# Kernel optimization log

Measured on AMD Instinct MI355X. Metric: run time of the kernel, lower is better.

## Reference

```python
import jax, jax.numpy as jnp
import numpy as np

B, L, D = 8, 128, 512
MAW = 8             # config.max_arg_width
SWF = 20            # config.span_width_feature_size
FF = 512            # config.ffnn_size
R = 19              # label_space_size - 1
G = 4               # gold predicates per sentence
SPAN = 3 * D + SWF  # span_emb_size = 1556


def setup_inputs() -> dict:
    key = jax.random.key(0)
    ks = jax.random.split(key, 30)
    w = lambda k, shape, s=0.02: (jax.random.normal(k, shape, dtype=jnp.float32) * s)
    z = lambda n: jnp.zeros((n,), jnp.float32)
    return {
        'hidden_states': jax.random.normal(ks[0], (B, L, D), dtype=jnp.float32),
        'sent_lengths': 64 + jax.random.randint(ks[1], (B,), 0, L - 64 + 1),
        'gold_predicates': jax.random.randint(ks[2], (B, G), 0, 64),
        'width_emb_table': w(ks[3], (MAW, SWF), 0.1),
        'arg_w0': w(ks[4], (SPAN, FF)), 'arg_b0': z(FF),
        'arg_w1': w(ks[5], (FF, FF)), 'arg_b1': z(FF),
        'arg_wp': w(ks[6], (FF, 1)), 'arg_bp': z(1),
        'pred_w0': w(ks[7], (D, FF)), 'pred_b0': z(FF),
        'pred_w1': w(ks[8], (FF, FF)), 'pred_b1': z(FF),
        'pred_wp': w(ks[9], (FF, 1)), 'pred_bp': z(1),
        'srl_w0': w(ks[10], (SPAN + D, FF)), 'srl_b0': z(FF),
        'srl_w1': w(ks[11], (FF, FF)), 'srl_b1': z(FF),
        'srl_wp': w(ks[12], (FF, R)), 'srl_bp': z(R),
        'scale_w': w(ks[13], (D, SPAN)), 'scale_b': z(SPAN),
        'biaffine_w': w(ks[14], (R, SPAN + 1, SPAN + 1), 0.005),
    }


def _ffn(x, w0, b0, w1, b1, wp, bp):
    # stacked Linear+ReLU (dropout = identity at inference) + projection
    h = jax.nn.relu(x @ w0 + b0)
    h = jax.nn.relu(h @ w1 + b1)
    return h @ wp + bp


def reference(hidden_states, sent_lengths, gold_predicates, width_emb_table,
              arg_w0, arg_b0, arg_w1, arg_b1, arg_wp, arg_bp,
              pred_w0, pred_b0, pred_w1, pred_b1, pred_wp, pred_bp,
              srl_w0, srl_b0, srl_w1, srl_b1, srl_wp, srl_bp,
              scale_w, scale_b, biaffine_w):
    S = L * MAW  # candidates per sentence
    # --- get_candidate_spans: note original flattening order is [width, start] ---
    starts = jnp.broadcast_to(jnp.arange(L), (B, MAW, L)).reshape(B, S)
    widths = jnp.broadcast_to(jnp.arange(MAW)[None, :, None], (B, MAW, L)).reshape(B, S)
    ends = starts + widths
    cand_mask = ends < sent_lengths[:, None]            # [B, S]
    starts = starts * cand_mask
    ends = ends * cand_mask
    # --- get_span_emb: gathers of start/end tokens, width embedding, head mean ---
    b_idx = jnp.arange(B)[:, None]
    start_emb = hidden_states[b_idx, starts]            # [B, S, D]
    end_emb = hidden_states[b_idx, ends]                # [B, S, D]
    width_idx = ends - starts                           # span_width - 1
    width_emb = width_emb_table[width_idx]              # [B, S, SWF]
    span_idx = jnp.clip(starts[:, :, None] + jnp.arange(MAW), 0, L - 1)  # [B, S, MAW]
    text_emb = hidden_states[jnp.arange(B)[:, None, None], span_idx]     # [B, S, MAW, D]
    idx_mask = (jnp.arange(MAW) <= width_idx[:, :, None]).astype(hidden_states.dtype)
    head_emb = jnp.mean(text_emb * idx_mask[..., None], axis=2)  # mean over MAW (as torch.mean)
    span_emb = jnp.concatenate([start_emb, end_emb, width_emb, head_emb], axis=-1)  # [B, S, SPAN]
    # --- arg unary scores ---
    arg_scores = _ffn(span_emb, arg_w0, arg_b0, arg_w1, arg_b1, arg_wp, arg_bp)[..., 0]  # [B, S]
    # --- gold predicates: gather token embeddings, pred unary scores ---
    pred_emb = hidden_states[b_idx, gold_predicates]    # [B, G, D]
    pred_scores = _ffn(pred_emb, pred_w0, pred_b0, pred_w1, pred_b1, pred_wp, pred_bp)[..., 0]  # [B, G]
    # --- SRL pairwise FFN on concat(span_emb, pred_emb); split first layer to avoid
    #     materializing the [B,S,G,SPAN+D] concat (same math) ---
    a = span_emb @ srl_w0[:SPAN]                        # [B, S, FF]
    p = pred_emb @ srl_w0[SPAN:]                        # [B, G, FF]
    h = jax.nn.relu(a[:, :, None, :] + p[:, None, :, :] + srl_b0)  # [B, S, G, FF]
    h = jax.nn.relu(h @ srl_w1 + srl_b1)
    srl_unary = h @ srl_wp + srl_bp                     # [B, S, G, R]
    # --- biaffine: predicate_scale FeedForward then bilinear with bias on both sides ---
    pred_scaled = jax.nn.relu(pred_emb @ scale_w + scale_b)  # [B, G, SPAN]
    ones_s = jnp.ones(span_emb.shape[:-1] + (1,), span_emb.dtype)
    ones_p = jnp.ones(pred_scaled.shape[:-1] + (1,), pred_scaled.dtype)
    span1 = jnp.concatenate([span_emb, ones_s], axis=-1)       # [B, S, SPAN+1]
    pred1 = jnp.concatenate([pred_scaled, ones_p], axis=-1)    # [B, G, SPAN+1]
    t = jnp.einsum('bgj,rij->bgri', pred1, biaffine_w)         # [B, G, R, SPAN+1]
    biaff = jnp.einsum('bsi,bgri->bsgr', span1, t)             # [B, S, G, R]
    scores = srl_unary + biaff + arg_scores[:, :, None, None] + pred_scores[:, None, :, None]
    # zero out pruned (invalid) candidate spans
    scores = scores * cand_mask[:, :, None, None].astype(scores.dtype)
    return scores
```

## Files before the change

kernel.cpp:

```cpp
#include <hip/hip_runtime.h>

constexpr int B_   = 8;
constexpr int L_   = 128;
constexpr int D_   = 512;
constexpr int MAW_ = 8;
constexpr int SWF_ = 20;
constexpr int FF_  = 512;
constexpr int R_   = 19;
constexpr int G_   = 4;
constexpr int SPAN_ = 3 * D_ + SWF_;
constexpr int S1_   = SPAN_ + 1;
constexpr int S_    = L_ * MAW_;
constexpr int NS_   = B_ * S_;
constexpr int NP_   = B_ * G_;
constexpr int TM_   = R_ * S1_;
constexpr int M8_   = NS_ * G_;

constexpr size_t OFF_HS_ARG = 0;
constexpr size_t OFF_HE_ARG = 524288;
constexpr size_t OFF_HH_ARG = 1048576;
constexpr size_t OFF_HS_SRL = 1572864;
constexpr size_t OFF_HE_SRL = 2097152;
constexpr size_t OFF_HH_SRL = 2621440;
constexpr size_t OFF_PH_ARG = 3145728;
constexpr size_t OFF_PH_SRL = 3674112;
constexpr size_t OFF_P_SRL  = 4202496;
constexpr size_t OFF_PSCORE = 4218880;
constexpr size_t OFF_PRED1  = 4218912;
constexpr size_t OFF_WD_ARG = 4268736;
constexpr size_t OFF_WD_SRL = 4272832;
constexpr size_t OFF_T      = 4276928;
constexpr size_t OFF_MS     = 5223584;
constexpr size_t OFF_ME     = 5301408;
constexpr size_t OFF_MHP    = 5379232;
constexpr size_t OFF_MW     = 5457664;
constexpr size_t OFF_TC     = 5462528;
constexpr size_t OFF_HARG   = 5463136;
constexpr size_t OFF_ASRL   = 9657440;
constexpr size_t OFF_ARGS   = 13851744;

__global__ __launch_bounds__(256) void k1_proj(const float* __restrict__ hidden,
                                               const float* __restrict__ arg_w0,
                                               const float* __restrict__ srl_w0,
                                               float* __restrict__ ws) {
  __shared__ float As[16][68];
  __shared__ float Bs[16][132];
  const int tid = threadIdx.x;
  const int m0 = blockIdx.x * 64;
  const int by = blockIdx.y;
  const int j = by >> 2;
  const int c0 = (by & 3) * 128;
  const int rowoffs[3] = {0, 512, 1044};
  const float* W = (j < 3) ? (arg_w0 + (size_t)rowoffs[j] * FF_)
                           : (srl_w0 + (size_t)rowoffs[j - 3] * FF_);
  float* C = ws + (size_t)j * 524288;

  const int tx = tid & 15, ty = tid >> 4;
  float acc[4][8];
#pragma unroll
  for (int i = 0; i < 4; ++i)
#pragma unroll
    for (int jj = 0; jj < 8; ++jj) acc[i][jj] = 0.f;

  const int mlA = tid >> 2, kqA = (tid & 3) * 4;
  const int n4B = (tid & 31) * 4, krB = tid >> 5;

  for (int kc = 0; kc < 32; ++kc) {
    float4 av = *(const float4*)&hidden[(size_t)(m0 + mlA) * D_ + kc * 16 + kqA];
    As[kqA + 0][mlA] = av.x; As[kqA + 1][mlA] = av.y;
    As[kqA + 2][mlA] = av.z; As[kqA + 3][mlA] = av.w;
#pragma unroll
    for (int it = 0; it < 2; ++it) {
      int k = krB + it * 8;
      *(float4*)&Bs[k][n4B] = *(const float4*)&W[(size_t)(kc * 16 + k) * FF_ + c0 + n4B];
    }
    __syncthreads();
#pragma unroll
    for (int kk = 0; kk < 16; ++kk) {
      float4 a  = *(const float4*)&As[kk][ty * 4];
      float4 b0 = *(const float4*)&Bs[kk][tx * 8];
      float4 b1 = *(const float4*)&Bs[kk][tx * 8 + 4];
      float ar[4] = {a.x, a.y, a.z, a.w};
      float br[8] = {b0.x, b0.y, b0.z, b0.w, b1.x, b1.y, b1.z, b1.w};
#pragma unroll
      for (int i = 0; i < 4; ++i)
#pragma unroll
        for (int jj = 0; jj < 8; ++jj) acc[i][jj] += ar[i] * br[jj];
    }
    __syncthreads();
  }
#pragma unroll
  for (int i = 0; i < 4; ++i) {
    int row = m0 + ty * 4 + i;
    float4 o0 = {acc[i][0], acc[i][1], acc[i][2], acc[i][3]};
    float4 o1 = {acc[i][4], acc[i][5], acc[i][6], acc[i][7]};
    *(float4*)&C[(size_t)row * FF_ + c0 + tx * 8] = o0;
    *(float4*)&C[(size_t)row * FF_ + c0 + tx * 8 + 4] = o1;
  }
}

__global__ __launch_bounds__(256) void k2_prefix(float* __restrict__ ws) {
  int idx = blockIdx.x * 256 + threadIdx.x;
  int mat = idx >> 12;
  int b = (idx >> 9) & 7;
  int f = idx & 511;
  const float* src = ws + (mat == 0 ? OFF_HH_ARG : OFF_HH_SRL) + (size_t)(b * L_) * D_ + f;
  float* dst = ws + (mat == 0 ? OFF_PH_ARG : OFF_PH_SRL) + (size_t)(b * (L_ + 1)) * D_ + f;
  float run = 0.f;
  dst[0] = 0.f;
  for (int l = 0; l < L_; ++l) {
    run += src[(size_t)l * D_];
    dst[(size_t)(l + 1) * D_] = run;
  }
}

__global__ __launch_bounds__(256) void k3a_pred(const float* __restrict__ hidden,
                                                const int* __restrict__ goldp,
                                                const float* __restrict__ pw0, const float* __restrict__ pb0,
                                                const float* __restrict__ pw1, const float* __restrict__ pb1,
                                                const float* __restrict__ pwp, const float* __restrict__ pbp,
                                                const float* __restrict__ srl_w0,
                                                float* __restrict__ ws) {
  __shared__ float emb[512], h0[512], h1[512], red[256];
  const int p = blockIdx.x, tid = threadIdx.x;
  const int b = p >> 2;
  const int pi = goldp[p];
  const float* hrow = hidden + (size_t)(b * L_ + pi) * D_;
  emb[tid] = hrow[tid];
  emb[tid + 256] = hrow[tid + 256];
  __syncthreads();
#pragma unroll
  for (int h = 0; h < 2; ++h) {
    int f = tid + h * 256;
    float a = pb0[f];
    for (int d = 0; d < D_; ++d) a += emb[d] * pw0[(size_t)d * FF_ + f];
    h0[f] = fmaxf(a, 0.f);
  }
  __syncthreads();
#pragma unroll
  for (int h = 0; h < 2; ++h) {
    int f = tid + h * 256;
    float a = pb1[f];
    for (int d = 0; d < FF_; ++d) a += h0[d] * pw1[(size_t)d * FF_ + f];
    h1[f] = fmaxf(a, 0.f);
  }
  __syncthreads();
  red[tid] = h1[tid] * pwp[tid] + h1[tid + 256] * pwp[tid + 256];
  __syncthreads();
  for (int s = 128; s > 0; s >>= 1) {
    if (tid < s) red[tid] += red[tid + s];
    __syncthreads();
  }
  if (tid == 0) ws[OFF_PSCORE + p] = red[0] + pbp[0];
#pragma unroll
  for (int h = 0; h < 2; ++h) {
    int f = tid + h * 256;
    float a = 0.f;
    for (int d = 0; d < D_; ++d) a += emb[d] * srl_w0[(size_t)(SPAN_ + d) * FF_ + f];
    ws[OFF_P_SRL + (size_t)p * FF_ + f] = a;
  }
}

__global__ __launch_bounds__(256) void k3b_scale(const float* __restrict__ hidden,
                                                 const int* __restrict__ goldp,
                                                 const float* __restrict__ scale_w,
                                                 const float* __restrict__ scale_b,
                                                 const float* __restrict__ wtab,
                                                 const float* __restrict__ arg_w0,
                                                 const float* __restrict__ srl_w0,
                                                 float* __restrict__ ws) {
  const int blk = blockIdx.x, tid = threadIdx.x;
  if (blk >= NP_ * 7) {
    int mat = blk - NP_ * 7;
    const float* W = (mat == 0 ? arg_w0 : srl_w0) + (size_t)(2 * D_) * FF_;
    float* dst = ws + (mat == 0 ? OFF_WD_ARG : OFF_WD_SRL);
    for (int idx = tid; idx < MAW_ * FF_; idx += 256) {
      int w = idx >> 9, f = idx & 511;
      float a = 0.f;
#pragma unroll
      for (int k = 0; k < SWF_; ++k) a += wtab[w * SWF_ + k] * W[(size_t)k * FF_ + f];
      dst[idx] = a;
    }
    return;
  }
  const int p = blk / 7, chunk = blk % 7;
  __shared__ float emb[512];
  const int b = p >> 2;
  const int pi = goldp[p];
  const float* hrow = hidden + (size_t)(b * L_ + pi) * D_;
  emb[tid] = hrow[tid];
  emb[tid + 256] = hrow[tid + 256];
  __syncthreads();
  const int i = chunk * 256 + tid;
  if (i < SPAN_) {
    float a = scale_b[i];
    for (int d = 0; d < D_; ++d) a += emb[d] * scale_w[(size_t)d * SPAN_ + i];
    ws[OFF_PRED1 + (size_t)p * S1_ + i] = fmaxf(a, 0.f);
  } else if (i == SPAN_) {
    ws[OFF_PRED1 + (size_t)p * S1_ + i] = 1.f;
  }
}

__global__ __launch_bounds__(256) void k4_t(const float* __restrict__ bw,
                                            float* __restrict__ ws) {
  __shared__ float As[32][65];
  __shared__ float Bs[32][36];
  const float* pred1 = ws + OFF_PRED1;
  float* t = ws + OFF_T;
  const int tid = threadIdx.x;
  const int m0 = blockIdx.x * 64;
  const int tx = tid & 7, ty = tid >> 3;
  float acc[2][4] = {{0.f, 0.f, 0.f, 0.f}, {0.f, 0.f, 0.f, 0.f}};
  const int mlA = tid >> 2, kqA = (tid & 3) * 8;
  const int pB = tid & 31, kqB = (tid >> 5) * 4;

  for (int kc = 0; kc < 49; ++kc) {
    const int j0 = kc * 32;
    {
      const int m = m0 + mlA;
      const bool mok = m < TM_;
      const float* arow = bw + (size_t)m * S1_ + j0 + kqA;
#pragma unroll
      for (int q = 0; q < 8; ++q) {
        int jj = j0 + kqA + q;
        As[kqA + q][mlA] = (mok && jj < S1_) ? arow[q] : 0.f;
      }
    }
    {
#pragma unroll
      for (int q = 0; q < 4; ++q) {
        int jj = j0 + kqB + q;
        Bs[kqB + q][pB] = (jj < S1_) ? pred1[(size_t)pB * S1_ + jj] : 0.f;
      }
    }
    __syncthreads();
#pragma unroll
    for (int kk = 0; kk < 32; ++kk) {
      float a0 = As[kk][ty * 2], a1 = As[kk][ty * 2 + 1];
      float4 bq = *(const float4*)&Bs[kk][tx * 4];
      acc[0][0] += a0 * bq.x; acc[0][1] += a0 * bq.y;
      acc[0][2] += a0 * bq.z; acc[0][3] += a0 * bq.w;
      acc[1][0] += a1 * bq.x; acc[1][1] += a1 * bq.y;
      acc[1][2] += a1 * bq.z; acc[1][3] += a1 * bq.w;
    }
    __syncthreads();
  }
#pragma unroll
  for (int i2 = 0; i2 < 2; ++i2) {
    int m = m0 + ty * 2 + i2;
    if (m < TM_) {
#pragma unroll
      for (int q = 0; q < 4; ++q) t[(size_t)(tx * 4 + q) * TM_ + m] = acc[i2][q];
    }
  }
}

__global__ __launch_bounds__(256) void k5_biaff(const float* __restrict__ hidden,
                                                const float* __restrict__ wtab,
                                                float* __restrict__ ws) {
  __shared__ float trow[S1_];
  __shared__ float mh[128];
  const int pr = blockIdx.x;
  const int p = pr / R_;
  const int b = p >> 2;
  const float* t = ws + OFF_T + (size_t)p * TM_ + (size_t)(pr % R_) * S1_;
  const int tid = threadIdx.x;
  for (int idx = tid; idx < S1_; idx += 256) trow[idx] = t[idx];
  __syncthreads();
  const int wv = tid >> 6, lane = tid & 63;
  const float* hb = hidden + (size_t)b * L_ * D_;
#pragma unroll
  for (int seg = 0; seg < 3; ++seg) {
    const int off = (seg == 0) ? 0 : (seg == 1) ? 512 : 1044;
    for (int l = wv * 32; l < wv * 32 + 32; ++l) {
      float part = 0.f;
#pragma unroll
      for (int q = 0; q < 8; ++q) {
        int d = q * 64 + lane;
        part += hb[(size_t)l * D_ + d] * trow[off + d];
      }
#pragma unroll
      for (int o = 32; o > 0; o >>= 1) part += __shfl_xor(part, o);
      if (lane == 0) {
        if (seg == 0) ws[OFF_MS + (size_t)pr * 128 + l] = part;
        else if (seg == 1) ws[OFF_ME + (size_t)pr * 128 + l] = part;
        else mh[l] = part;
      }
    }
  }
  __syncthreads();
  if (tid == 0) {
    float run = 0.f;
    float* Mhp = ws + OFF_MHP + (size_t)pr * 129;
    Mhp[0] = 0.f;
    for (int l = 0; l < 128; ++l) { run += mh[l]; Mhp[l + 1] = run; }
    ws[OFF_TC + pr] = trow[1556];
  }
  if (tid < MAW_) {
    float a = 0.f;
#pragma unroll
    for (int k = 0; k < SWF_; ++k) a += wtab[tid * SWF_ + k] * trow[1024 + k];
    ws[OFF_MW + (size_t)pr * 8 + tid] = a;
  }
}

__global__ __launch_bounds__(256) void k6_span(const int* __restrict__ slen,
                                               const float* __restrict__ arg_b0,
                                               const float* __restrict__ arg_bp,
                                               const float* __restrict__ srl_bp,
                                               float* __restrict__ ws,
                                               float* __restrict__ out) {
  const int sp = blockIdx.x, tid = threadIdx.x;
  const int b = sp >> 10, s = sp & 1023;
  const int w = s >> 7, l = s & 127;
  const bool valid = (l + w) < slen[b];
  const int st = valid ? l : 0;
  const int en = valid ? l + w : 0;
  const int wd = en - st;

  const float* HsA = ws + OFF_HS_ARG + (size_t)(b * 128 + st) * 512;
  const float* HeA = ws + OFF_HE_ARG + (size_t)(b * 128 + en) * 512;
  const float* PA1 = ws + OFF_PH_ARG + (size_t)(b * 129 + en + 1) * 512;
  const float* PA0 = ws + OFF_PH_ARG + (size_t)(b * 129 + st) * 512;
  const float* WdA = ws + OFF_WD_ARG + (size_t)wd * 512;
  const float* HsS = ws + OFF_HS_SRL + (size_t)(b * 128 + st) * 512;
  const float* HeS = ws + OFF_HE_SRL + (size_t)(b * 128 + en) * 512;
  const float* PS1 = ws + OFF_PH_SRL + (size_t)(b * 129 + en + 1) * 512;
  const float* PS0 = ws + OFF_PH_SRL + (size_t)(b * 129 + st) * 512;
  const float* WdS = ws + OFF_WD_SRL + (size_t)wd * 512;
  float* ha = ws + OFF_HARG + (size_t)sp * 512;
  float* as = ws + OFF_ASRL + (size_t)sp * 512;

#pragma unroll
  for (int h = 0; h < 2; ++h) {
    int f = tid + h * 256;
    float va = HsA[f] + HeA[f] + WdA[f] + (PA1[f] - PA0[f]) * 0.125f + arg_b0[f];
    ha[f] = fmaxf(va, 0.f);
    as[f] = HsS[f] + HeS[f] + WdS[f] + (PS1[f] - PS0[f]) * 0.125f;
  }
  if (tid == 0) ws[OFF_ARGS + sp] = arg_bp[0];
  if (tid < G_ * R_) {
    int g = tid / R_, r = tid % R_;
    out[((size_t)sp * G_ + g) * R_ + r] = srl_bp[r];
  }
}

__global__ __launch_bounds__(256) void k7_arg(const float* __restrict__ w1,
                                              const float* __restrict__ b1,
                                              const float* __restrict__ wp,
                                              float* __restrict__ ws) {
  __shared__ float As[16][136];
  __shared__ float Bs[16][132];
  __shared__ float wps[128];
  const float* A = ws + OFF_HARG;
  float* scores = ws + OFF_ARGS;
  const int tid = threadIdx.x;
  const int m0 = blockIdx.x * 128, n0 = blockIdx.y * 128;
  if (tid < 128) wps[tid] = wp[n0 + tid];
  const int tx = tid & 15, ty = tid >> 4;
  float acc[8][8];
#pragma unroll
  for (int i = 0; i < 8; ++i)
#pragma unroll
    for (int jj = 0; jj < 8; ++jj) acc[i][jj] = 0.f;
  const int mlA = tid >> 1, khA = (tid & 1) * 8;
  const int n4B = (tid & 31) * 4, krB = tid >> 5;

  for (int kc = 0; kc < 32; ++kc) {
    {
      const float* ar = &A[(size_t)(m0 + mlA) * 512 + kc * 16 + khA];
      float4 x0 = *(const float4*)ar, x1 = *(const float4*)(ar + 4);
      As[khA + 0][mlA] = x0.x; As[khA + 1][mlA] = x0.y;
      As[khA + 2][mlA] = x0.z; As[khA + 3][mlA] = x0.w;
      As[khA + 4][mlA] = x1.x; As[khA + 5][mlA] = x1.y;
      As[khA + 6][mlA] = x1.z; As[khA + 7][mlA] = x1.w;
    }
#pragma unroll
    for (int it = 0; it < 2; ++it) {
      int k = krB + it * 8;
      *(float4*)&Bs[k][n4B] = *(const float4*)&w1[(size_t)(kc * 16 + k) * 512 + n0 + n4B];
    }
    __syncthreads();
#pragma unroll
    for (int kk = 0; kk < 16; ++kk) {
      float4 a0 = *(const float4*)&As[kk][ty * 8];
      float4 a1 = *(const float4*)&As[kk][ty * 8 + 4];
      float4 v0 = *(const float4*)&Bs[kk][tx * 8];
      float4 v1 = *(const float4*)&Bs[kk][tx * 8 + 4];
      float ar[8] = {a0.x, a0.y, a0.z, a0.w, a1.x, a1.y, a1.z, a1.w};
      float br[8] = {v0.x, v0.y, v0.z, v0.w, v1.x, v1.y, v1.z, v1.w};
#pragma unroll
      for (int i = 0; i < 8; ++i)
#pragma unroll
        for (int jj = 0; jj < 8; ++jj) acc[i][jj] += ar[i] * br[jj];
    }
    __syncthreads();
  }
  float bj[8];
#pragma unroll
  for (int jj = 0; jj < 8; ++jj) bj[jj] = b1[n0 + tx * 8 + jj];
#pragma unroll
  for (int i = 0; i < 8; ++i) {
    float part = 0.f;
#pragma unroll
    for (int jj = 0; jj < 8; ++jj)
      part += fmaxf(acc[i][jj] + bj[jj], 0.f) * wps[tx * 8 + jj];
#pragma unroll
    for (int o = 1; o < 16; o <<= 1) part += __shfl_xor(part, o);
    if (tx == 0) atomicAdd(&scores[m0 + ty * 8 + i], part);
  }
}

__global__ __launch_bounds__(256) void k8_srl(const float* __restrict__ w1,
                                              const float* __restrict__ b1,
                                              const float* __restrict__ wp,
                                              const float* __restrict__ b0,
                                              float* __restrict__ ws,
                                              float* __restrict__ out) {
  __shared__ float As[16][136];
  __shared__ float Bs[16][132];
  __shared__ float wps[128 * 19];
  const float* a_srl = ws + OFF_ASRL;
  const float* p_srl = ws + OFF_P_SRL;
  const int tid = threadIdx.x;
  const int m0 = blockIdx.x * 128, n0 = blockIdx.y * 128;
  for (int idx = tid; idx < 128 * 19; idx += 256) wps[idx] = wp[(size_t)n0 * 19 + idx];
  const int tx = tid & 15, ty = tid >> 4;
  float acc[8][8];
#pragma unroll
  for (int i = 0; i < 8; ++i)
#pragma unroll
    for (int jj = 0; jj < 8; ++jj) acc[i][jj] = 0.f;
  const int mlA = tid >> 1, khA = (tid & 1) * 8;
  const int m = m0 + mlA;
  const int sprow = m >> 2;
  const int prow = ((m >> 12) << 2) | (m & 3);
  const float* arow = a_srl + (size_t)sprow * 512;
  const float* prp = p_srl + (size_t)prow * 512;
  const int n4B = (tid & 31) * 4, krB = tid >> 5;

  for (int kc = 0; kc < 32; ++kc) {
    {
      const int kb = kc * 16 + khA;
      float4 x0 = *(const float4*)&arow[kb], x1 = *(const float4*)&arow[kb + 4];
      float4 y0 = *(const float4*)&prp[kb], y1 = *(const float4*)&prp[kb + 4];
      float4 z0 = *(const float4*)&b0[kb], z1 = *(const float4*)&b0[kb + 4];
      As[khA + 0][mlA] = fmaxf(x0.x + y0.x + z0.x, 0.f);
      As[khA + 1][mlA] = fmaxf(x0.y + y0.y + z0.y, 0.f);
      As[khA + 2][mlA] = fmaxf(x0.z + y0.z + z0.z, 0.f);
      As[khA + 3][mlA] = fmaxf(x0.w + y0.w + z0.w, 0.f);
      As[khA + 4][mlA] = fmaxf(x1.x + y1.x + z1.x, 0.f);
      As[khA + 5][mlA] = fmaxf(x1.y + y1.y + z1.y, 0.f);
      As[khA + 6][mlA] = fmaxf(x1.z + y1.z + z1.z, 0.f);
      As[khA + 7][mlA] = fmaxf(x1.w + y1.w + z1.w, 0.f);
    }
#pragma unroll
    for (int it = 0; it < 2; ++it) {
      int k = krB + it * 8;
      *(float4*)&Bs[k][n4B] = *(const float4*)&w1[(size_t)(kc * 16 + k) * 512 + n0 + n4B];
    }
    __syncthreads();
#pragma unroll
    for (int kk = 0; kk < 16; ++kk) {
      float4 a0 = *(const float4*)&As[kk][ty * 8];
      float4 a1 = *(const float4*)&As[kk][ty * 8 + 4];
      float4 v0 = *(const float4*)&Bs[kk][tx * 8];
      float4 v1 = *(const float4*)&Bs[kk][tx * 8 + 4];
      float ar[8] = {a0.x, a0.y, a0.z, a0.w, a1.x, a1.y, a1.z, a1.w};
      float br[8] = {v0.x, v0.y, v0.z, v0.w, v1.x, v1.y, v1.z, v1.w};
#pragma unroll
      for (int i = 0; i < 8; ++i)
#pragma unroll
        for (int jj = 0; jj < 8; ++jj) acc[i][jj] += ar[i] * br[jj];
    }
    __syncthreads();
  }
  float bj[8];
#pragma unroll
  for (int jj = 0; jj < 8; ++jj) bj[jj] = b1[n0 + tx * 8 + jj];
#pragma unroll
  for (int i = 0; i < 8; ++i) {
    float pr_[19];
#pragma unroll
    for (int r = 0; r < 19; ++r) pr_[r] = 0.f;
#pragma unroll
    for (int jj = 0; jj < 8; ++jj) {
      float v = fmaxf(acc[i][jj] + bj[jj], 0.f);
      const float* wrow = &wps[(tx * 8 + jj) * 19];
#pragma unroll
      for (int r = 0; r < 19; ++r) pr_[r] += v * wrow[r];
    }
#pragma unroll
    for (int o = 1; o < 16; o <<= 1) {
#pragma unroll
      for (int r = 0; r < 19; ++r) pr_[r] += __shfl_xor(pr_[r], o);
    }
    if (tx == 0) {
      size_t row = (size_t)(m0 + ty * 8 + i);
#pragma unroll
      for (int r = 0; r < 19; ++r) atomicAdd(&out[row * 19 + r], pr_[r]);
    }
  }
}

__global__ __launch_bounds__(128) void k9_fin(const int* __restrict__ slen,
                                              float* __restrict__ out,
                                              const float* __restrict__ ws) {
  const int sp = blockIdx.x, tid = threadIdx.x;
  if (tid >= G_ * R_) return;
  const int b = sp >> 10, s = sp & 1023;
  const int w = s >> 7, l = s & 127;
  const bool valid = (l + w) < slen[b];
  const int st = valid ? l : 0;
  const int en = valid ? l + w : 0;
  const int wd = en - st;
  const int g = tid / R_, r = tid % R_;
  const int p = b * G_ + g;
  const int pr = p * R_ + r;
  const size_t o = ((size_t)sp * G_ + g) * R_ + r;
  float val = out[o]
            + ws[OFF_MS + (size_t)pr * 128 + st]
            + ws[OFF_ME + (size_t)pr * 128 + en]
            + ws[OFF_MW + (size_t)pr * 8 + wd]
            + (ws[OFF_MHP + (size_t)pr * 129 + en + 1] - ws[OFF_MHP + (size_t)pr * 129 + st]) * 0.125f
            + ws[OFF_TC + pr]
            + ws[OFF_ARGS + sp]
            + ws[OFF_PSCORE + p];
  out[o] = valid ? val : 0.f;
}

extern "C" void kernel_launch(void* const* d_in, const int* in_sizes, int n_in,
                              void* d_out, int out_size, void* d_ws, size_t ws_size,
                              hipStream_t stream) {
  const float* hidden  = (const float*)d_in[0];
  const int*   slen    = (const int*)d_in[1];
  const int*   goldp   = (const int*)d_in[2];
  const float* wtab    = (const float*)d_in[3];
  const float* arg_w0  = (const float*)d_in[4];
  const float* arg_b0  = (const float*)d_in[5];
  const float* arg_w1  = (const float*)d_in[6];
  const float* arg_b1  = (const float*)d_in[7];
  const float* arg_wp  = (const float*)d_in[8];
  const float* arg_bp  = (const float*)d_in[9];
  const float* pred_w0 = (const float*)d_in[10];
  const float* pred_b0 = (const float*)d_in[11];
  const float* pred_w1 = (const float*)d_in[12];
  const float* pred_b1 = (const float*)d_in[13];
  const float* pred_wp = (const float*)d_in[14];
  const float* pred_bp = (const float*)d_in[15];
  const float* srl_w0  = (const float*)d_in[16];
  const float* srl_b0  = (const float*)d_in[17];
  const float* srl_w1  = (const float*)d_in[18];
  const float* srl_b1  = (const float*)d_in[19];
  const float* srl_wp  = (const float*)d_in[20];
  const float* srl_bp  = (const float*)d_in[21];
  const float* scale_w = (const float*)d_in[22];
  const float* scale_b = (const float*)d_in[23];
  const float* bw      = (const float*)d_in[24];
  float* out = (float*)d_out;
  float* ws  = (float*)d_ws;

  k1_proj<<<dim3(16, 24), 256, 0, stream>>>(hidden, arg_w0, srl_w0, ws);
  k2_prefix<<<32, 256, 0, stream>>>(ws);
  k3a_pred<<<32, 256, 0, stream>>>(hidden, goldp, pred_w0, pred_b0, pred_w1, pred_b1,
                                   pred_wp, pred_bp, srl_w0, ws);
  k3b_scale<<<NP_ * 7 + 2, 256, 0, stream>>>(hidden, goldp, scale_w, scale_b, wtab,
                                             arg_w0, srl_w0, ws);
  k4_t<<<(TM_ + 63) / 64, 256, 0, stream>>>(bw, ws);
  k5_biaff<<<NP_ * R_, 256, 0, stream>>>(hidden, wtab, ws);
  k6_span<<<NS_, 256, 0, stream>>>(slen, arg_b0, arg_bp, srl_bp, ws, out);
  k7_arg<<<dim3(NS_ / 128, 4), 256, 0, stream>>>(arg_w1, arg_b1, arg_wp, ws);
  k8_srl<<<dim3(M8_ / 128, 4), 256, 0, stream>>>(srl_w1, srl_b1, srl_wp, srl_b0, ws, out);
  k9_fin<<<NS_, 128, 0, stream>>>(slen, out, ws);
}
```

Baseline: 1.152 ms.

## Use bf16 MFMA for arg and SRL hidden-layer GEMMs with transposed bf16 weights

Adds a kernel that converts and transposes arg_w1 and srl_w1 into bf16 in workspace. k6 now stores the arg hidden activations as bf16. k7 and k8 are rewritten to use 16x16x32 bf16 MFMA tiles instead of FP32 FMA register tiles. The k8 epilogue is reorganised around a 20-wide padded projection weight. This targets the FP32 compute cost of the two large GEMMs (32K x 512 x 512) but lowers the precision of the hidden activations and weights to bf16.

```diff
diff --git a/kernel.cpp b/kernel.cpp
--- a/kernel.cpp
+++ b/kernel.cpp
@@ -36,8 +36,19 @@
 constexpr size_t OFF_MW     = 5457664;
 constexpr size_t OFF_TC     = 5462528;
 constexpr size_t OFF_HARG   = 5463136;
+constexpr size_t OFF_W1T_ARG = 7560288;
+constexpr size_t OFF_W1T_SRL = 7691360;
 constexpr size_t OFF_ASRL   = 9657440;
 constexpr size_t OFF_ARGS   = 13851744;
+
+typedef short bf16x8 __attribute__((ext_vector_type(8)));
+typedef float f32x4  __attribute__((ext_vector_type(4)));
+
+__device__ __forceinline__ unsigned short f2bf(float x) {
+  unsigned u = __float_as_uint(x);
+  unsigned r = (u + 0x7FFFu + ((u >> 16) & 1u)) >> 16;
+  return (unsigned short)r;
+}
 
 __global__ __launch_bounds__(256) void k1_proj(const float* __restrict__ hidden,
                                                const float* __restrict__ arg_w0,
@@ -97,6 +108,37 @@
     *(float4*)&C[(size_t)row * FF_ + c0 + tx * 8] = o0;
     *(float4*)&C[(size_t)row * FF_ + c0 + tx * 8 + 4] = o1;
   }
+}
+
+__global__ __launch_bounds__(256) void kw_cvt(const float* __restrict__ arg_w1,
+                                              const float* __restrict__ srl_w1,
+                                              float* __restrict__ ws) {
+  __shared__ float tile[64][65];
+  const int mat = blockIdx.z;
+  const float* W = mat ? srl_w1 : arg_w1;
+  unsigned short* T = (unsigned short*)(ws + (mat ? OFF_W1T_SRL : OFF_W1T_ARG));
+  const int k0 = blockIdx.x * 64, n0 = blockIdx.y * 64;
+  const int t = threadIdx.x;
+  const int kk = t >> 4, nn = (t & 15) * 4;
+#pragma unroll
+  for (int it = 0; it < 4; ++it) {
+    float4 v = *(const float4*)&W[(size_t)(k0 + kk + it * 16) * 512 + n0 + nn];
+    tile[kk + it * 16][nn + 0] = v.x; tile[kk + it * 16][nn + 1] = v.y;
+    tile[kk + it * 16][nn + 2] = v.z; tile[kk + it * 16][nn + 3] = v.w;
+  }
+  __syncthreads();
+  const int n = t >> 2, kc = (t & 3) * 16;
+  unsigned o[8];
+#pragma unroll
+  for (int j2 = 0; j2 < 8; ++j2) {
+    unsigned lo = f2bf(tile[kc + 2 * j2][n]);
+    unsigned hi = f2bf(tile[kc + 2 * j2 + 1][n]);
+    o[j2] = lo | (hi << 16);
+  }
+  uint4 u0 = {o[0], o[1], o[2], o[3]}, u1 = {o[4], o[5], o[6], o[7]};
+  unsigned short* dst = &T[(size_t)(n0 + n) * 512 + k0 + kc];
+  *(uint4*)dst = u0;
+  *(uint4*)(dst + 8) = u1;
 }
 
 __global__ __launch_bounds__(256) void k2_prefix(float* __restrict__ ws) {
@@ -328,14 +370,14 @@
   const float* PS1 = ws + OFF_PH_SRL + (size_t)(b * 129 + en + 1) * 512;
   const float* PS0 = ws + OFF_PH_SRL + (size_t)(b * 129 + st) * 512;
   const float* WdS = ws + OFF_WD_SRL + (size_t)wd * 512;
-  float* ha = ws + OFF_HARG + (size_t)sp * 512;
+  unsigned short* ha = (unsigned short*)(ws + OFF_HARG) + (size_t)sp * 512;
   float* as = ws + OFF_ASRL + (size_t)sp * 512;
 
 #pragma unroll
   for (int h = 0; h < 2; ++h) {
     int f = tid + h * 256;
     float va = HsA[f] + HeA[f] + WdA[f] + (PA1[f] - PA0[f]) * 0.125f + arg_b0[f];
-    ha[f] = fmaxf(va, 0.f);
+    ha[f] = f2bf(fmaxf(va, 0.f));
     as[f] = HsS[f] + HeS[f] + WdS[f] + (PS1[f] - PS0[f]) * 0.125f;
   }
   if (tid == 0) ws[OFF_ARGS + sp] = arg_bp[0];
@@ -345,160 +387,184 @@
   }
 }
 
-__global__ __launch_bounds__(256) void k7_arg(const float* __restrict__ w1,
-                                              const float* __restrict__ b1,
+__global__ __launch_bounds__(256) void k7_arg(const float* __restrict__ b1,
                                               const float* __restrict__ wp,
                                               float* __restrict__ ws) {
-  __shared__ float As[16][136];
-  __shared__ float Bs[16][132];
+  __shared__ short As[128 * 40];
+  __shared__ short Bs[128 * 40];
   __shared__ float wps[128];
-  const float* A = ws + OFF_HARG;
+  __shared__ float bs1[128];
+  const unsigned short* Aall = (const unsigned short*)(ws + OFF_HARG);
+  const unsigned short* Ball = (const unsigned short*)(ws + OFF_W1T_ARG);
   float* scores = ws + OFF_ARGS;
   const int tid = threadIdx.x;
   const int m0 = blockIdx.x * 128, n0 = blockIdx.y * 128;
-  if (tid < 128) wps[tid] = wp[n0 + tid];
-  const int tx = tid & 15, ty = tid >> 4;
-  float acc[8][8];
-#pragma unroll
-  for (int i = 0; i < 8; ++i)
-#pragma unroll
-    for (int jj = 0; jj < 8; ++jj) acc[i][jj] = 0.f;
-  const int mlA = tid >> 1, khA = (tid & 1) * 8;
-  const int n4B = (tid & 31) * 4, krB = tid >> 5;
-
-  for (int kc = 0; kc < 32; ++kc) {
+  if (tid < 128) { wps[tid] = wp[n0 + tid]; bs1[tid] = b1[n0 + tid]; }
+  const int lane = tid & 63, wv = tid >> 6;
+  const int wr = wv >> 1, wc = wv & 1;
+  const int col = lane & 15, kg = lane >> 4;
+  const int sm = tid >> 1, sh = tid & 1;
+  const int bn = tid >> 2, bc = tid & 3;
+  f32x4 acc[4][4];
+#pragma unroll
+  for (int i = 0; i < 4; ++i)
+#pragma unroll
+    for (int j = 0; j < 4; ++j) {
+      acc[i][j][0] = 0.f; acc[i][j][1] = 0.f; acc[i][j][2] = 0.f; acc[i][j][3] = 0.f;
+    }
+
+  for (int kc = 0; kc < 16; ++kc) {
     {
-      const float* ar = &A[(size_t)(m0 + mlA) * 512 + kc * 16 + khA];
-      float4 x0 = *(const float4*)ar, x1 = *(const float4*)(ar + 4);
-      As[khA + 0][mlA] = x0.x; As[khA + 1][mlA] = x0.y;
-      As[khA + 2][mlA] = x0.z; As[khA + 3][mlA] = x0.w;
-      As[khA + 4][mlA] = x1.x; As[khA + 5][mlA] = x1.y;
-      As[khA + 6][mlA] = x1.z; As[khA + 7][mlA] = x1.w;
+      const unsigned short* src = &Aall[(size_t)(m0 + sm) * 512 + kc * 32 + sh * 16];
+      *(uint4*)&As[sm * 40 + sh * 16] = *(const uint4*)src;
+      *(uint4*)&As[sm * 40 + sh * 16 + 8] = *(const uint4*)(src + 8);
     }
 #pragma unroll
     for (int it = 0; it < 2; ++it) {
-      int k = krB + it * 8;
-      *(float4*)&Bs[k][n4B] = *(const float4*)&w1[(size_t)(kc * 16 + k) * 512 + n0 + n4B];
-    }
-    __syncthreads();
-#pragma unroll
-    for (int kk = 0; kk < 16; ++kk) {
-      float4 a0 = *(const float4*)&As[kk][ty * 8];
-      float4 a1 = *(const float4*)&As[kk][ty * 8 + 4];
-      float4 v0 = *(const float4*)&Bs[kk][tx * 8];
-      float4 v1 = *(const float4*)&Bs[kk][tx * 8 + 4];
-      float ar[8] = {a0.x, a0.y, a0.z, a0.w, a1.x, a1.y, a1.z, a1.w};
-      float br[8] = {v0.x, v0.y, v0.z, v0.w, v1.x, v1.y, v1.z, v1.w};
-#pragma unroll
-      for (int i = 0; i < 8; ++i)
-#pragma unroll
-        for (int jj = 0; jj < 8; ++jj) acc[i][jj] += ar[i] * br[jj];
-    }
-    __syncthreads();
-  }
-  float bj[8];
-#pragma unroll
-  for (int jj = 0; jj < 8; ++jj) bj[jj] = b1[n0 + tx * 8 + jj];
-#pragma unroll
-  for (int i = 0; i < 8; ++i) {
-    float part = 0.f;
-#pragma unroll
-    for (int jj = 0; jj < 8; ++jj)
-      part += fmaxf(acc[i][jj] + bj[jj], 0.f) * wps[tx * 8 + jj];
-#pragma unroll
-    for (int o = 1; o < 16; o <<= 1) part += __shfl_xor(part, o);
-    if (tx == 0) atomicAdd(&scores[m0 + ty * 8 + i], part);
-  }
-}
-
-__global__ __launch_bounds__(256) void k8_srl(const float* __restrict__ w1,
-                                              const float* __restrict__ b1,
+      const int n = bn + it * 64;
+      *(uint4*)&Bs[n * 40 + bc * 8] =
+          *(const uint4*)&Ball[(size_t)(n0 + n) * 512 + kc * 32 + bc * 8];
+    }
+    __syncthreads();
+    bf16x8 bfr[4], afr[4];
+#pragma unroll
+    for (int nf = 0; nf < 4; ++nf)
+      bfr[nf] = *(const bf16x8*)&Bs[(wc * 64 + nf * 16 + col) * 40 + kg * 8];
+#pragma unroll
+    for (int mf = 0; mf < 4; ++mf)
+      afr[mf] = *(const bf16x8*)&As[(wr * 64 + mf * 16 + col) * 40 + kg * 8];
+#pragma unroll
+    for (int nf = 0; nf < 4; ++nf)
+#pragma unroll
+      for (int mf = 0; mf < 4; ++mf)
+        acc[nf][mf] = __builtin_amdgcn_mfma_f32_16x16x32_bf16(bfr[nf], afr[mf], acc[nf][mf], 0, 0, 0);
+    __syncthreads();
+  }
+#pragma unroll
+  for (int mf = 0; mf < 4; ++mf) {
+    float s = 0.f;
+#pragma unroll
+    for (int nf = 0; nf < 4; ++nf)
+#pragma unroll
+      for (int q = 0; q < 4; ++q) {
+        const int nloc = wc * 64 + nf * 16 + kg * 4 + q;
+        s += fmaxf(acc[nf][mf][q] + bs1[nloc], 0.f) * wps[nloc];
+      }
+    s += __shfl_xor(s, 16);
+    s += __shfl_xor(s, 32);
+    if (kg == 0) atomicAdd(&scores[m0 + wr * 64 + mf * 16 + col], s);
+  }
+}
+
+__global__ __launch_bounds__(256) void k8_srl(const float* __restrict__ b1,
                                               const float* __restrict__ wp,
                                               const float* __restrict__ b0,
                                               float* __restrict__ ws,
                                               float* __restrict__ out) {
-  __shared__ float As[16][136];
-  __shared__ float Bs[16][132];
-  __shared__ float wps[128 * 19];
+  __shared__ short As[128 * 40];
+  __shared__ short Bs[128 * 40];
+  __shared__ float wps20[128 * 20];
+  __shared__ float bs1[128];
   const float* a_srl = ws + OFF_ASRL;
   const float* p_srl = ws + OFF_P_SRL;
+  const unsigned short* Ball = (const unsigned short*)(ws + OFF_W1T_SRL);
   const int tid = threadIdx.x;
   const int m0 = blockIdx.x * 128, n0 = blockIdx.y * 128;
-  for (int idx = tid; idx < 128 * 19; idx += 256) wps[idx] = wp[(size_t)n0 * 19 + idx];
-  const int tx = tid & 15, ty = tid >> 4;
-  float acc[8][8];
-#pragma unroll
-  for (int i = 0; i < 8; ++i)
-#pragma unroll
-    for (int jj = 0; jj < 8; ++jj) acc[i][jj] = 0.f;
-  const int mlA = tid >> 1, khA = (tid & 1) * 8;
-  const int m = m0 + mlA;
-  const int sprow = m >> 2;
-  const int prow = ((m >> 12) << 2) | (m & 3);
-  const float* arow = a_srl + (size_t)sprow * 512;
-  const float* prp = p_srl + (size_t)prow * 512;
-  const int n4B = (tid & 31) * 4, krB = tid >> 5;
-
-  for (int kc = 0; kc < 32; ++kc) {
+  for (int idx = tid; idx < 128 * 20; idx += 256) {
+    int n = idx / 20, r = idx - n * 20;
+    wps20[idx] = (r < 19) ? wp[(size_t)(n0 + n) * 19 + r] : 0.f;
+  }
+  if (tid < 128) bs1[tid] = b1[n0 + tid];
+  const int lane = tid & 63, wv = tid >> 6;
+  const int wr = wv >> 1, wc = wv & 1;
+  const int col = lane & 15, kg = lane >> 4;
+  const int sm = tid >> 1, sh = tid & 1;
+  const int gm = m0 + sm;
+  const float* arow = a_srl + (size_t)(gm >> 2) * 512;
+  const float* prow = p_srl + (size_t)(((gm >> 12) << 2) | (gm & 3)) * 512;
+  const int bn = tid >> 2, bc = tid & 3;
+  f32x4 acc[4][4];
+#pragma unroll
+  for (int i = 0; i < 4; ++i)
+#pragma unroll
+    for (int j = 0; j < 4; ++j) {
+      acc[i][j][0] = 0.f; acc[i][j][1] = 0.f; acc[i][j][2] = 0.f; acc[i][j][3] = 0.f;
+    }
+
+  for (int kc = 0; kc < 16; ++kc) {
     {
-      const int kb = kc * 16 + khA;
-      float4 x0 = *(const float4*)&arow[kb], x1 = *(const float4*)&arow[kb + 4];
-      float4 y0 = *(const float4*)&prp[kb], y1 = *(const float4*)&prp[kb + 4];
-      float4 z0 = *(const float4*)&b0[kb], z1 = *(const float4*)&b0[kb + 4];
-      As[khA + 0][mlA] = fmaxf(x0.x + y0.x + z0.x, 0.f);
-      As[khA + 1][mlA] = fmaxf(x0.y + y0.y + z0.y, 0.f);
-      As[khA + 2][mlA] = fmaxf(x0.z + y0.z + z0.z, 0.f);
-      As[khA + 3][mlA] = fmaxf(x0.w + y0.w + z0.w, 0.f);
-      As[khA + 4][mlA] = fmaxf(x1.x + y1.x + z1.x, 0.f);
-      As[khA + 5][mlA] = fmaxf(x1.y + y1.y + z1.y, 0.f);
-      As[khA + 6][mlA] = fmaxf(x1.z + y1.z + z1.z, 0.f);
-      As[khA + 7][mlA] = fmaxf(x1.w + y1.w + z1.w, 0.f);
+      const int kb = kc * 32 + sh * 16;
+      unsigned uo[8];
+#pragma unroll
+      for (int q4 = 0; q4 < 4; ++q4) {
+        float4 xa = *(const float4*)&arow[kb + q4 * 4];
+        float4 xp = *(const float4*)&prow[kb + q4 * 4];
+        float4 xb = *(const float4*)&b0[kb + q4 * 4];
+        float v0 = fmaxf(xa.x + xp.x + xb.x, 0.f);
+        float v1 = fmaxf(xa.y + xp.y + xb.y, 0.f);
+        float v2 = fmaxf(xa.z + xp.z + xb.z, 0.f);
+        float v3 = fmaxf(xa.w + xp.w + xb.w, 0.f);
+        uo[q4 * 2 + 0] = (unsigned)f2bf(v0) | ((unsigned)f2bf(v1) << 16);
+        uo[q4 * 2 + 1] = (unsigned)f2bf(v2) | ((unsigned)f2bf(v3) << 16);
+      }
+      uint4 w0 = {uo[0], uo[1], uo[2], uo[3]}, w1v = {uo[4], uo[5], uo[6], uo[7]};
+      *(uint4*)&As[sm * 40 + sh * 16] = w0;
+      *(uint4*)&As[sm * 40 + sh * 16 + 8] = w1v;
     }
 #pragma unroll
     for (int it = 0; it < 2; ++it) {
-      int k = krB + it * 8;
-      *(float4*)&Bs[k][n4B] = *(const float4*)&w1[(size_t)(kc * 16 + k) * 512 + n0 + n4B];
-    }
-    __syncthreads();
-#pragma unroll
-    for (int kk = 0; kk < 16; ++kk) {
-      float4 a0 = *(const float4*)&As[kk][ty * 8];
-      float4 a1 = *(const float4*)&As[kk][ty * 8 + 4];
-      float4 v0 = *(const float4*)&Bs[kk][tx * 8];
-      float4 v1 = *(const float4*)&Bs[kk][tx * 8 + 4];
-      float ar[8] = {a0.x, a0.y, a0.z, a0.w, a1.x, a1.y, a1.z, a1.w};
-      float br[8] = {v0.x, v0.y, v0.z, v0.w, v1.x, v1.y, v1.z, v1.w};
-#pragma unroll
-      for (int i = 0; i < 8; ++i)
-#pragma unroll
-        for (int jj = 0; jj < 8; ++jj) acc[i][jj] += ar[i] * br[jj];
-    }
-    __syncthreads();
-  }
-  float bj[8];
-#pragma unroll
-  for (int jj = 0; jj < 8; ++jj) bj[jj] = b1[n0 + tx * 8 + jj];
-#pragma unroll
-  for (int i = 0; i < 8; ++i) {
-    float pr_[19];
-#pragma unroll
-    for (int r = 0; r < 19; ++r) pr_[r] = 0.f;
-#pragma unroll
-    for (int jj = 0; jj < 8; ++jj) {
-      float v = fmaxf(acc[i][jj] + bj[jj], 0.f);
-      const float* wrow = &wps[(tx * 8 + jj) * 19];
-#pragma unroll
-      for (int r = 0; r < 19; ++r) pr_[r] += v * wrow[r];
-    }
-#pragma unroll
-    for (int o = 1; o < 16; o <<= 1) {
-#pragma unroll
-      for (int r = 0; r < 19; ++r) pr_[r] += __shfl_xor(pr_[r], o);
-    }
-    if (tx == 0) {
-      size_t row = (size_t)(m0 + ty * 8 + i);
-#pragma unroll
-      for (int r = 0; r < 19; ++r) atomicAdd(&out[row * 19 + r], pr_[r]);
+      const int n = bn + it * 64;
+      *(uint4*)&Bs[n * 40 + bc * 8] =
+          *(const uint4*)&Ball[(size_t)(n0 + n) * 512 + kc * 32 + bc * 8];
+    }
+    __syncthreads();
+    bf16x8 bfr[4], afr[4];
+#pragma unroll
+    for (int nf = 0; nf < 4; ++nf)
+      bfr[nf] = *(const bf16x8*)&Bs[(wc * 64 + nf * 16 + col) * 40 + kg * 8];
+#pragma unroll
+    for (int mf = 0; mf < 4; ++mf)
+      afr[mf] = *(const bf16x8*)&As[(wr * 64 + mf * 16 + col) * 40 + kg * 8];
+#pragma unroll
+    for (int nf = 0; nf < 4; ++nf)
+#pragma unroll
+      for (int mf = 0; mf < 4; ++mf)
+        acc[nf][mf] = __builtin_amdgcn_mfma_f32_16x16x32_bf16(bfr[nf], afr[mf], acc[nf][mf], 0, 0, 0);
+    __syncthreads();
+  }
+  float pr[4][20];
+#pragma unroll
+  for (int mf = 0; mf < 4; ++mf)
+#pragma unroll
+    for (int r = 0; r < 20; ++r) pr[mf][r] = 0.f;
+#pragma unroll
+  for (int nf = 0; nf < 4; ++nf)
+#pragma unroll
+    for (int q = 0; q < 4; ++q) {
+      const int nloc = wc * 64 + nf * 16 + kg * 4 + q;
+      const float bb = bs1[nloc];
+      float w4[20];
+#pragma unroll
+      for (int c = 0; c < 5; ++c) {
+        float4 v = *(const float4*)&wps20[nloc * 20 + c * 4];
+        w4[c * 4 + 0] = v.x; w4[c * 4 + 1] = v.y; w4[c * 4 + 2] = v.z; w4[c * 4 + 3] = v.w;
+      }
+#pragma unroll
+      for (int mf = 0; mf < 4; ++mf) {
+        const float val = fmaxf(acc[nf][mf][q] + bb, 0.f);
+#pragma unroll
+        for (int r = 0; r < 20; ++r) pr[mf][r] += val * w4[r];
+      }
+    }
+#pragma unroll
+  for (int mf = 0; mf < 4; ++mf) {
+    const size_t row = (size_t)(m0 + wr * 64 + mf * 16 + col);
+#pragma unroll
+    for (int r = 0; r < 19; ++r) {
+      float v = pr[mf][r];
+      v += __shfl_xor(v, 16);
+      v += __shfl_xor(v, 32);
+      if (kg == 0) atomicAdd(&out[row * 19 + r], v);
     }
   }
 }
@@ -560,6 +626,7 @@
   float* out = (float*)d_out;
   float* ws  = (float*)d_ws;
 
+  kw_cvt<<<dim3(8, 8, 2), 256, 0, stream>>>(arg_w1, srl_w1, ws);
   k1_proj<<<dim3(16, 24), 256, 0, stream>>>(hidden, arg_w0, srl_w0, ws);
   k2_prefix<<<32, 256, 0, stream>>>(ws);
   k3a_pred<<<32, 256, 0, stream>>>(hidden, goldp, pred_w0, pred_b0, pred_w1, pred_b1,
@@ -569,7 +636,7 @@
   k4_t<<<(TM_ + 63) / 64, 256, 0, stream>>>(bw, ws);
   k5_biaff<<<NP_ * R_, 256, 0, stream>>>(hidden, wtab, ws);
   k6_span<<<NS_, 256, 0, stream>>>(slen, arg_b0, arg_bp, srl_bp, ws, out);
-  k7_arg<<<dim3(NS_ / 128, 4), 256, 0, stream>>>(arg_w1, arg_b1, arg_wp, ws);
-  k8_srl<<<dim3(M8_ / 128, 4), 256, 0, stream>>>(srl_w1, srl_b1, srl_wp, srl_b0, ws, out);
+  k7_arg<<<dim3(64, 4), 256, 0, stream>>>(arg_b1, arg_wp, ws);
+  k8_srl<<<dim3(256, 4), 256, 0, stream>>>(srl_b1, srl_wp, srl_b0, ws, out);
   k9_fin<<<NS_, 128, 0, stream>>>(slen, out, ws);
 }
```

Result: no change. 1.142 ms (-0.9%).
